# Kernel optimization log

Hardware: AMD Instinct MI355X
Metric: run time of the kernel (lower is better)

Reference implementation:

```python
import jax, jax.numpy as jnp
import numpy as np

K = 40        # nearest neighbors
BN_EPS = 1e-5  # nn.BatchNorm1d default eps


def _bn(x, g, b):
    # training-mode BatchNorm1d: batch mean, biased variance
    mu = x.mean(0)
    var = x.var(0)
    return g * (x - mu) / jnp.sqrt(var + BN_EPS) + b


def setup_inputs() -> dict:
    key = jax.random.key(0)
    ks = jax.random.split(key, 16)
    N, Cin, D, S, P = 8192, 16, 32, 3, 32

    def w(k, i, o):
        return jax.random.normal(k, (i, o), jnp.float32) * (1.0 / np.sqrt(i))

    return {
        "x": jax.random.normal(ks[0], (N, Cin), jnp.float32),
        "original_coords": jax.random.normal(ks[1], (N, 3), jnp.float32),
        "batch": jnp.zeros((N,), jnp.int32),
        "step_count": 0,
        "num_layer": 1,
        # pre_gravnet MLP
        "pre_w1": w(ks[2], Cin, D), "pre_b1": jnp.zeros((D,), jnp.float32),
        "pre_w2": w(ks[3], D, D), "pre_b2": jnp.zeros((D,), jnp.float32),
        "bn1_g": jnp.ones((D,), jnp.float32), "bn1_b": jnp.zeros((D,), jnp.float32),
        # GravNetConv projections
        "lin_s_w": w(ks[4], D, S),
        "lin_h_w": w(ks[5], D, P), "lin_h_b": jnp.zeros((P,), jnp.float32),
        "lin_w": w(ks[6], D + 2 * P, D), "lin_b": jnp.zeros((D,), jnp.float32),
        # post_gravnet MLP (in = out_channels + space_dims + d_shape = 32+3+32)
        "post_w1": w(ks[7], D + S + D, D), "post_b1": jnp.zeros((D,), jnp.float32),
        "post_w2": w(ks[8], D, D), "post_b2": jnp.zeros((D,), jnp.float32),
        "bn2_g": jnp.ones((D,), jnp.float32), "bn2_b": jnp.zeros((D,), jnp.float32),
    }


def reference(x, original_coords, batch, step_count, num_layer,
              pre_w1, pre_b1, pre_w2, pre_b2, bn1_g, bn1_b,
              lin_s_w, lin_h_w, lin_h_b, lin_w, lin_b,
              post_w1, post_b1, post_w2, post_b2, bn2_g, bn2_b):
    N = x.shape[0]

    # pre_gravnet MLP + batchnorm
    h = jax.nn.elu(x @ pre_w1 + pre_b1)
    h = jax.nn.elu(h @ pre_w2 + pre_b2)
    x_in = _bn(h, bn1_g, bn1_b)

    # GravNetConv projections
    h_l = x_in @ lin_h_w + lin_h_b          # [N, P] propagated features
    s_l = x_in @ lin_s_w                    # [N, S] learned coordinate space

    # kNN graph in s-space (self loops excluded)
    sq = jnp.sum(s_l * s_l, axis=1)
    d2 = sq[:, None] + sq[None, :] - 2.0 * (s_l @ s_l.T)   # [N, N]
    d2 = jnp.maximum(d2, 0.0)
    d2 = jnp.where(jnp.eye(N, dtype=bool), jnp.inf, d2)
    _, idx = jax.lax.top_k(-d2, K)           # [N, K] neighbor indices

    # per-edge squared distance (NOTE: propagate uses the SQUARED distance,
    # faithful to the source where edge_weight is never re-bound to sqrt)
    edge_sq = jnp.take_along_axis(d2, idx, axis=1)    # [N, K]
    dist = jnp.sqrt(edge_sq + 1e-6)                   # [N, K]

    # DGL-side reductions at dst = edge_index[1] = neighbor index
    dst = idx.reshape(-1)
    distf = dist.reshape(-1)
    indeg = jax.ops.segment_sum(jnp.ones_like(distf), dst, num_segments=N)
    sum_d = jax.ops.segment_sum(distf, dst, num_segments=N)
    avdist = jnp.where(indeg > 0, sum_d / jnp.maximum(indeg, 1.0), 0.0)
    loss_regularizing_neig = 0.01 * jnp.mean(jnp.square(avdist - 0.5))

    norm_d = distf / (sum_d + 1e-4)[dst]              # EdgeWeightNorm('right')
    # faithful to source bug: '_edge_w_gndist' is set to the NORMALIZED dist,
    # and apply_edges multiplies by the RAW '_edge_w'
    degs2 = jax.ops.segment_sum(norm_d, dst, num_segments=N) + 1e-4
    gn_final = distf / degs2[dst]
    loss_llregulariser = 0.1 * jnp.mean(jnp.square(norm_d - gn_final))

    # message passing: msg = h_l[neighbor] * squared_dist, mean+max over the
    # K neighbors of each source node (regular fan-in -> dense reduce)
    msgs = h_l[idx] * edge_sq[..., None]              # [N, K, P]
    agg = jnp.concatenate([msgs.mean(1), msgs.max(1)], axis=-1)  # [N, 2P]
    xgn = jnp.concatenate([agg, x_in], axis=-1) @ lin_w + lin_b   # [N, 32]

    # post_gravnet MLP + batchnorm
    cat = jnp.concatenate([xgn, s_l, x_in], axis=1)   # [N, 67]
    o = jax.nn.elu(cat @ post_w1 + post_b1)
    o = jax.nn.elu(o @ post_w2 + post_b2)
    out = _bn(o, bn2_g, bn2_b)
    return (out, loss_regularizing_neig, loss_llregulariser)
```

## Files before the change

kernel.cpp:

```cpp
#include <hip/hip_runtime.h>
#include <math.h>

#define NPTS 8192
#define KNN 40
#define DD 32
#define CIN 16
#define RPB 8
#define QPB 8
#define QTR 2048
#define CAP3 64

#define OFF_H      0u
#define OFF_XIN    262144u
#define OFF_HL     524288u
#define OFF_SL     786432u
#define OFF_ESQ    819200u
#define OFF_O      1146880u
#define OFF_IDX    1409024u
#define OFF_SUMD   1736704u
#define OFF_INDEG  1744896u
#define OFF_STATS  1753088u
#define ZERO_FLOATS (8192u + 8192u + 130u * 32u)

#define ST(i) stats[(i) * 32]

__device__ __forceinline__ float elu_f(float x) { return x > 0.f ? x : (expf(x) - 1.f); }

__device__ __forceinline__ float grp_sum32(float v) {
#pragma unroll
    for (int m = 1; m < 32; m <<= 1) v += __shfl_xor(v, m);
    return v;
}

__device__ __forceinline__ unsigned fkey(float x) {
    unsigned b = __float_as_uint(x);
    return b ^ ((unsigned)((int)b >> 31) | 0x80000000u);
}
__device__ __forceinline__ float kinv(unsigned k) {
    unsigned b = (k & 0x80000000u) ? (k ^ 0x80000000u) : ~k;
    return __uint_as_float(b);
}

__device__ __forceinline__ unsigned bisect_kth4(unsigned u0, unsigned u1,
    unsigned u2, unsigned u3, int kth) {
    unsigned lo = 0u, hi = 0xFFFFFFFFu;
    while (lo < hi) {
        unsigned mid = lo + ((hi - lo) >> 1);
        int cnt = __popcll(__ballot(u0 <= mid)) + __popcll(__ballot(u1 <= mid))
                + __popcll(__ballot(u2 <= mid)) + __popcll(__ballot(u3 <= mid));
        if (cnt >= kth) hi = mid; else lo = mid + 1;
    }
    return hi;
}

__global__ __launch_bounds__(256) void k_pre(const float* __restrict__ x,
    const float* __restrict__ w1, const float* __restrict__ b1,
    const float* __restrict__ w2, const float* __restrict__ b2,
    float* __restrict__ h, float* __restrict__ stats)
{
    __shared__ float sw1[CIN * DD], sw2[DD * DD], sb1[DD], sb2[DD];
    __shared__ float bufx[RPB][20], buft[RPB][36];
    __shared__ float sstat[2 * DD];
    int tid = threadIdx.x;
    for (int t = tid; t < CIN * DD; t += 256) sw1[t] = w1[t];
    for (int t = tid; t < DD * DD; t += 256) sw2[t] = w2[t];
    if (tid < DD) { sb1[tid] = b1[tid]; sb2[tid] = b2[tid]; }
    if (tid < 2 * DD) sstat[tid] = 0.f;

    int r = tid >> 5, ch = tid & 31;
    int g = blockIdx.x * RPB + r;
    if (ch < CIN) bufx[r][ch] = x[(size_t)g * CIN + ch];
    __syncthreads();

    float acc = sb1[ch];
#pragma unroll
    for (int k4 = 0; k4 < CIN; k4 += 4) {
        float4 v = *(const float4*)&bufx[r][k4];
        acc = fmaf(v.x, sw1[(k4 + 0) * DD + ch], acc);
        acc = fmaf(v.y, sw1[(k4 + 1) * DD + ch], acc);
        acc = fmaf(v.z, sw1[(k4 + 2) * DD + ch], acc);
        acc = fmaf(v.w, sw1[(k4 + 3) * DD + ch], acc);
    }
    acc = elu_f(acc);
    buft[r][ch] = acc;
    __syncthreads();

    float o = sb2[ch];
#pragma unroll
    for (int k4 = 0; k4 < DD; k4 += 4) {
        float4 v = *(const float4*)&buft[r][k4];
        o = fmaf(v.x, sw2[(k4 + 0) * DD + ch], o);
        o = fmaf(v.y, sw2[(k4 + 1) * DD + ch], o);
        o = fmaf(v.z, sw2[(k4 + 2) * DD + ch], o);
        o = fmaf(v.w, sw2[(k4 + 3) * DD + ch], o);
    }
    o = elu_f(o);
    h[(size_t)g * DD + ch] = o;

    float s = o + __shfl_xor(o, 32);
    float q = o * o;
    q += __shfl_xor(q, 32);
    if ((tid & 32) == 0) { atomicAdd(&sstat[ch], s); atomicAdd(&sstat[DD + ch], q); }
    __syncthreads();
    if (tid < 2 * DD) atomicAdd(&ST(tid), sstat[tid]);
}

__global__ __launch_bounds__(256) void k_proj(const float* __restrict__ h,
    const float* __restrict__ stats,
    const float* __restrict__ g1, const float* __restrict__ b1g,
    const float* __restrict__ hw, const float* __restrict__ hb,
    const float* __restrict__ sw,
    float* __restrict__ xin, float* __restrict__ hl, float4* __restrict__ sl4)
{
    __shared__ float shw[DD * DD], ssw[DD * 3], sa[DD], sbp[DD], shb[DD];
    __shared__ float rrow[RPB][36];
    int tid = threadIdx.x;
    for (int t = tid; t < DD * DD; t += 256) shw[t] = hw[t];
    if (tid < DD * 3) ssw[tid] = sw[tid];
    if (tid < DD) {
        float mean = ST(tid) * (1.f / NPTS);
        float var = ST(32 + tid) * (1.f / NPTS) - mean * mean;
        float a = g1[tid] * rsqrtf(var + 1e-5f);
        sa[tid] = a;
        sbp[tid] = b1g[tid] - a * mean;
        shb[tid] = hb[tid];
    }
    __syncthreads();

    int r = tid >> 5, ch = tid & 31;
    int g = blockIdx.x * RPB + r;

    float v = fmaf(sa[ch], h[(size_t)g * DD + ch], sbp[ch]);
    xin[(size_t)g * DD + ch] = v;
    rrow[r][ch] = v;

    float p0 = v * ssw[ch * 3 + 0];
    float p1 = v * ssw[ch * 3 + 1];
    float p2 = v * ssw[ch * 3 + 2];
    p0 = grp_sum32(p0); p1 = grp_sum32(p1); p2 = grp_sum32(p2);
    if (ch == 0) sl4[g] = make_float4(p0, p1, p2, 0.5f * (p0 * p0 + p1 * p1 + p2 * p2));
    __syncthreads();

    float o = shb[ch];
#pragma unroll
    for (int k4 = 0; k4 < DD; k4 += 4) {
        float4 vv = *(const float4*)&rrow[r][k4];
        o = fmaf(vv.x, shw[(k4 + 0) * DD + ch], o);
        o = fmaf(vv.y, shw[(k4 + 1) * DD + ch], o);
        o = fmaf(vv.z, shw[(k4 + 2) * DD + ch], o);
        o = fmaf(vv.w, shw[(k4 + 3) * DD + ch], o);
    }
    hl[(size_t)g * DD + ch] = o;
}

__device__ __forceinline__ void emit_one(unsigned u, int j, float qw,
    unsigned thr, int nlt, int need, int prelt, int preeq,
    unsigned long long mlt, unsigned long long meq, unsigned long long ltm,
    int rb, int* __restrict__ idxo, float* __restrict__ esq,
    float* __restrict__ sumd, float* __restrict__ indeg)
{
    int pos = -1;
    if (u < thr) pos = prelt + __popcll(mlt & ltm);
    else if (u == thr) {
        int rk = preeq + __popcll(meq & ltm);
        if (rk < need) pos = nlt + rk;
    }
    if (pos >= 0) {
        float e = kinv(u);
        float d2 = fmaxf(2.f * (e + qw), 0.f);
        idxo[rb + pos] = j; esq[rb + pos] = d2;
        float dist = sqrtf(d2 + 1e-6f);
        atomicAdd(&sumd[j], dist); atomicAdd(&indeg[j], 1.f);
    }
}

__device__ __forceinline__ void select_emit4(
    const float2* b0, int c0, const float2* b1, int c1,
    const float2* b2, int c2, const float2* b3, int c3,
    int qidx, float qw, int lane,
    int* __restrict__ idxo, float* __restrict__ esq,
    float* __restrict__ sumd, float* __restrict__ indeg)
{
    float e0 = INFINITY, e1 = INFINITY, e2 = INFINITY, e3 = INFINITY;
    int j0 = -1, j1 = -1, j2 = -1, j3 = -1;
    if (lane < c0) { float2 t = b0[lane]; e0 = t.x; j0 = __float_as_int(t.y); }
    if (lane < c1) { float2 t = b1[lane]; e1 = t.x; j1 = __float_as_int(t.y); }
    if (lane < c2) { float2 t = b2[lane]; e2 = t.x; j2 = __float_as_int(t.y); }
    if (lane < c3) { float2 t = b3[lane]; e3 = t.x; j3 = __float_as_int(t.y); }
    if (j0 == qidx) e0 = INFINITY;
    if (j1 == qidx) e1 = INFINITY;
    if (j2 == qidx) e2 = INFINITY;
    if (j3 == qidx) e3 = INFINITY;
    unsigned u0 = fkey(e0), u1 = fkey(e1), u2 = fkey(e2), u3 = fkey(e3);
    unsigned thr = bisect_kth4(u0, u1, u2, u3, KNN);
    unsigned long long ltm = (1ull << lane) - 1;
    unsigned long long mlt0 = __ballot(u0 < thr), mlt1 = __ballot(u1 < thr);
    unsigned long long mlt2 = __ballot(u2 < thr), mlt3 = __ballot(u3 < thr);
    unsigned long long meq0 = __ballot(u0 == thr), meq1 = __ballot(u1 == thr);
    unsigned long long meq2 = __ballot(u2 == thr), meq3 = __ballot(u3 == thr);
    int n0 = __popcll(mlt0), n1 = __popcll(mlt1), n2 = __popcll(mlt2), n3 = __popcll(mlt3);
    int q0 = __popcll(meq0), q1 = __popcll(meq1), q2 = __popcll(meq2);
    int nlt = n0 + n1 + n2 + n3;
    int need = KNN - nlt;
    int rb = qidx * KNN;

    emit_one(u0, j0, qw, thr, nlt, need, 0, 0, mlt0, meq0, ltm, rb, idxo, esq, sumd, indeg);
    emit_one(u1, j1, qw, thr, nlt, need, n0, q0, mlt1, meq1, ltm, rb, idxo, esq, sumd, indeg);
    emit_one(u2, j2, qw, thr, nlt, need, n0 + n1, q0 + q1, mlt2, meq2, ltm, rb, idxo, esq, sumd, indeg);
    emit_one(u3, j3, qw, thr, nlt, need, n0 + n1 + n2, q0 + q1 + q2, mlt3, meq3, ltm, rb, idxo, esq, sumd, indeg);
}

#define EDIST8(pt, q) fmaf(-qx[q], (pt).x, fmaf(-qy[q], (pt).y, fmaf(-qz[q], (pt).z, (pt).w)))

__global__ __launch_bounds__(256) void k_knn(const float4* __restrict__ sl4,
    int* __restrict__ idxo, float* __restrict__ esq,
    float* __restrict__ sumd, float* __restrict__ indeg)
{
    __shared__ float pool[QPB][4][64];
    __shared__ float2 cand[QPB][4][CAP3];
    __shared__ int cnts[QPB][4];
    __shared__ float sthr[QPB];
    int tid = threadIdx.x, lane = tid & 63, w = tid >> 6;
    int qbase = blockIdx.x * QPB;

    float qx[QPB], qy[QPB], qz[QPB];
#pragma unroll
    for (int q = 0; q < QPB; ++q) {
        float4 t = sl4[qbase + q];
        qx[q] = t.x; qy[q] = t.y; qz[q] = t.z;
    }
    int pbase = w * QTR;
    int rot = blockIdx.x & (QTR / 64 - 1);

    float m0[QPB];
#pragma unroll
    for (int q = 0; q < QPB; ++q) m0[q] = INFINITY;

    for (int i = 0; i < QTR / 64; ++i) {
        int chunk = (i + rot) & (QTR / 64 - 1);
        float4 pt = sl4[pbase + chunk * 64 + lane];
#pragma unroll
        for (int q = 0; q < QPB; ++q) m0[q] = fminf(m0[q], EDIST8(pt, q));
    }
#pragma unroll
    for (int q = 0; q < QPB; ++q) pool[q][w][lane] = m0[q];
    __syncthreads();

#pragma unroll
    for (int k = 0; k < 2; ++k) {
        int q = 2 * w + k;
        unsigned t = bisect_kth4(fkey(pool[q][0][lane]), fkey(pool[q][1][lane]),
                                 fkey(pool[q][2][lane]), fkey(pool[q][3][lane]), KNN + 1);
        if (lane == 0) sthr[q] = kinv(t);
    }
    __syncthreads();

    float thr[QPB];
#pragma unroll
    for (int q = 0; q < QPB; ++q) thr[q] = sthr[q];

    unsigned long long ltm = (1ull << lane) - 1;
    int cnt[QPB];
#pragma unroll
    for (int q = 0; q < QPB; ++q) cnt[q] = 0;

    for (int i = 0; i < QTR / 64; ++i) {
        int chunk = (i + rot) & (QTR / 64 - 1);
        int jj = pbase + chunk * 64 + lane;
        float4 pt = sl4[jj];
#pragma unroll
        for (int q = 0; q < QPB; ++q) {
            float e = EDIST8(pt, q);
            unsigned long long mm = __ballot(e <= thr[q]);
            if (mm) {
                if (e <= thr[q]) {
                    int pos = cnt[q] + __popcll(mm & ltm);
                    if (pos < CAP3) cand[q][w][pos] = make_float2(e, __int_as_float(jj));
                }
                cnt[q] += __popcll(mm);
            }
        }
    }
    if (lane == 0) {
#pragma unroll
        for (int q = 0; q < QPB; ++q) cnts[q][w] = cnt[q] < CAP3 ? cnt[q] : CAP3;
    }
    __syncthreads();

#pragma unroll
    for (int k = 0; k < 2; ++k) {
        int q = 2 * w + k;
        int qi = qbase + q;
        float qw_ = sl4[qi].w;
        select_emit4(cand[q][0], cnts[q][0], cand[q][1], cnts[q][1],
                     cand[q][2], cnts[q][2], cand[q][3], cnts[q][3],
                     qi, qw_, lane, idxo, esq, sumd, indeg);
    }
}

__global__ __launch_bounds__(256) void k_agg(
    const int* __restrict__ idx, const float* __restrict__ esq,
    const float* __restrict__ hl, const float* __restrict__ xin,
    const float4* __restrict__ sl4,
    const float* __restrict__ sumd, const float* __restrict__ indeg,
    const float* __restrict__ lw, const float* __restrict__ lb,
    const float* __restrict__ pw1, const float* __restrict__ pb1,
    const float* __restrict__ pw2, const float* __restrict__ pb2,
    float* __restrict__ o, float* __restrict__ stats)
{
    __shared__ float slw[96 * DD], spw1[67 * DD], spw2[DD * DD];
    __shared__ float slb[DD], spb1[DD], spb2[DD];
    __shared__ float rbuf[RPB][100];
    __shared__ float rb2[RPB][68];
    __shared__ float sstat[2 * DD];
    __shared__ float sl1, sl2;
    int tid = threadIdx.x;
    for (int t = tid; t < 96 * DD; t += 256) slw[t] = lw[t];
    for (int t = tid; t < 67 * DD; t += 256) spw1[t] = pw1[t];
    for (int t = tid; t < DD * DD; t += 256) spw2[t] = pw2[t];
    if (tid < DD) { slb[tid] = lb[tid]; spb1[tid] = pb1[tid]; spb2[tid] = pb2[tid]; }
    if (tid < 2 * DD) sstat[tid] = 0.f;
    if (tid == 254) sl1 = 0.f;
    if (tid == 255) sl2 = 0.f;

    int r = tid >> 5, ch = tid & 31;
    int g = blockIdx.x * RPB + r;
    int rb = g * KNN;

    float sv = 0.f, mv = -INFINITY;
#pragma unroll 8
    for (int k = 0; k < KNN; ++k) {
        int j = idx[rb + k];
        float w = esq[rb + k];
        float m = hl[(size_t)j * DD + ch] * w;
        sv += m;
        mv = fmaxf(mv, m);
    }
    rbuf[r][ch] = sv * (1.f / KNN);
    rbuf[r][32 + ch] = mv;
    rbuf[r][64 + ch] = xin[(size_t)g * DD + ch];
    if (ch == 0) { float4 s = sl4[g]; rbuf[r][96] = s.x; rbuf[r][97] = s.y; rbuf[r][98] = s.z; }
    __syncthreads();

    float l2 = 0.f;
    {
        int j = idx[rb + ch];
        float w = esq[rb + ch];
        float dist = sqrtf(w + 1e-6f);
        float sd = sumd[j];
        float r1 = 1.f / (sd + 1e-4f);
        float dg = sd * r1 + 1e-4f;
        float df = dist * r1 - dist / dg;
        l2 = df * df;
        if (ch < KNN - 32) {
            j = idx[rb + 32 + ch];
            w = esq[rb + 32 + ch];
            dist = sqrtf(w + 1e-6f);
            sd = sumd[j];
            r1 = 1.f / (sd + 1e-4f);
            dg = sd * r1 + 1e-4f;
            df = dist * r1 - dist / dg;
            l2 += df * df;
        }
    }
    l2 = grp_sum32(l2);
    if (ch == 0) {
        float id = indeg[g], sdg = sumd[g];
        float av = id > 0.f ? sdg / fmaxf(id, 1.f) : 0.f;
        float dd = av - 0.5f;
        atomicAdd(&sl2, l2);
        atomicAdd(&sl1, dd * dd);
    }

    float acc = slb[ch];
#pragma unroll
    for (int k4 = 0; k4 < 96; k4 += 4) {
        float4 v = *(const float4*)&rbuf[r][k4];
        acc = fmaf(v.x, slw[(k4 + 0) * DD + ch], acc);
        acc = fmaf(v.y, slw[(k4 + 1) * DD + ch], acc);
        acc = fmaf(v.z, slw[(k4 + 2) * DD + ch], acc);
        acc = fmaf(v.w, slw[(k4 + 3) * DD + ch], acc);
    }
    rb2[r][ch] = acc;
    __syncthreads();

    acc = spb1[ch];
#pragma unroll
    for (int k4 = 0; k4 < DD; k4 += 4) {
        float4 v = *(const float4*)&rb2[r][k4];
        acc = fmaf(v.x, spw1[(k4 + 0) * DD + ch], acc);
        acc = fmaf(v.y, spw1[(k4 + 1) * DD + ch], acc);
        acc = fmaf(v.z, spw1[(k4 + 2) * DD + ch], acc);
        acc = fmaf(v.w, spw1[(k4 + 3) * DD + ch], acc);
    }
#pragma unroll
    for (int s2 = 0; s2 < 3; ++s2)
        acc = fmaf(rbuf[r][96 + s2], spw1[(32 + s2) * DD + ch], acc);
#pragma unroll
    for (int k4 = 0; k4 < DD; k4 += 4) {
        float4 v = *(const float4*)&rbuf[r][64 + k4];
        acc = fmaf(v.x, spw1[(35 + k4 + 0) * DD + ch], acc);
        acc = fmaf(v.y, spw1[(35 + k4 + 1) * DD + ch], acc);
        acc = fmaf(v.z, spw1[(35 + k4 + 2) * DD + ch], acc);
        acc = fmaf(v.w, spw1[(35 + k4 + 3) * DD + ch], acc);
    }
    acc = elu_f(acc);
    rb2[r][32 + ch] = acc;
    __syncthreads();

    acc = spb2[ch];
#pragma unroll
    for (int k4 = 0; k4 < DD; k4 += 4) {
        float4 v = *(const float4*)&rb2[r][32 + k4];
        acc = fmaf(v.x, spw2[(k4 + 0) * DD + ch], acc);
        acc = fmaf(v.y, spw2[(k4 + 1) * DD + ch], acc);
        acc = fmaf(v.z, spw2[(k4 + 2) * DD + ch], acc);
        acc = fmaf(v.w, spw2[(k4 + 3) * DD + ch], acc);
    }
    acc = elu_f(acc);
    o[(size_t)g * DD + ch] = acc;

    float s = acc + __shfl_xor(acc, 32);
    float q = acc * acc;
    q += __shfl_xor(q, 32);
    if ((tid & 32) == 0) { atomicAdd(&sstat[ch], s); atomicAdd(&sstat[DD + ch], q); }
    __syncthreads();
    if (tid < 2 * DD) atomicAdd(&ST(64 + tid), sstat[tid]);
    if (tid == 0) { atomicAdd(&ST(128), sl1); atomicAdd(&ST(129), sl2); }
}

__global__ __launch_bounds__(256) void k_out(const float* __restrict__ o,
    const float* __restrict__ stats, const float* __restrict__ g,
    const float* __restrict__ b, float* __restrict__ dout)
{
    __shared__ float sa[DD], sb[DD];
    int tid = threadIdx.x;
    if (tid < DD) {
        float mean = ST(64 + tid) * (1.f / NPTS);
        float var = ST(96 + tid) * (1.f / NPTS) - mean * mean;
        float a = g[tid] * rsqrtf(var + 1e-5f);
        sa[tid] = a;
        sb[tid] = b[tid] - a * mean;
    }
    __syncthreads();

    int t = blockIdx.x * 256 + tid;
    float4 v = ((const float4*)o)[t];
    int cbase = (t * 4) & (DD - 1);
    float4 rr;
    rr.x = fmaf(sa[cbase + 0], v.x, sb[cbase + 0]);
    rr.y = fmaf(sa[cbase + 1], v.y, sb[cbase + 1]);
    rr.z = fmaf(sa[cbase + 2], v.z, sb[cbase + 2]);
    rr.w = fmaf(sa[cbase + 3], v.w, sb[cbase + 3]);
    ((float4*)dout)[t] = rr;

    if (blockIdx.x == 0) {
        if (tid == DD)     dout[NPTS * DD]     = 0.01f * ST(128) * (1.f / NPTS);
        if (tid == DD + 1) dout[NPTS * DD + 1] = 0.1f  * ST(129) * (1.f / ((float)NPTS * KNN));
    }
}

extern "C" void kernel_launch(void* const* d_in, const int* in_sizes, int n_in,
                              void* d_out, int out_size, void* d_ws, size_t ws_size,
                              hipStream_t stream)
{
    (void)in_sizes; (void)n_in; (void)out_size; (void)ws_size;
    const float* x      = (const float*)d_in[0];
    const float* pre_w1 = (const float*)d_in[5];
    const float* pre_b1 = (const float*)d_in[6];
    const float* pre_w2 = (const float*)d_in[7];
    const float* pre_b2 = (const float*)d_in[8];
    const float* bn1_g  = (const float*)d_in[9];
    const float* bn1_b  = (const float*)d_in[10];
    const float* lin_s_w = (const float*)d_in[11];
    const float* lin_h_w = (const float*)d_in[12];
    const float* lin_h_b = (const float*)d_in[13];
    const float* lin_w   = (const float*)d_in[14];
    const float* lin_b   = (const float*)d_in[15];
    const float* post_w1 = (const float*)d_in[16];
    const float* post_b1 = (const float*)d_in[17];
    const float* post_w2 = (const float*)d_in[18];
    const float* post_b2 = (const float*)d_in[19];
    const float* bn2_g   = (const float*)d_in[20];
    const float* bn2_b   = (const float*)d_in[21];

    float* W = (float*)d_ws;
    float* h     = W + OFF_H;
    float* xin   = W + OFF_XIN;
    float* hl    = W + OFF_HL;
    float4* sl4  = (float4*)(W + OFF_SL);
    float* esq   = W + OFF_ESQ;
    float* o     = W + OFF_O;
    int*   idx   = (int*)(W + OFF_IDX);
    float* sumd  = W + OFF_SUMD;
    float* indeg = W + OFF_INDEG;
    float* stats = W + OFF_STATS;
    float* dout  = (float*)d_out;

    hipMemsetAsync(W + OFF_SUMD, 0, ZERO_FLOATS * sizeof(float), stream);

    k_pre<<<NPTS / RPB, 256, 0, stream>>>(x, pre_w1, pre_b1, pre_w2, pre_b2, h, stats);
    k_proj<<<NPTS / RPB, 256, 0, stream>>>(h, stats, bn1_g, bn1_b,
                                           lin_h_w, lin_h_b, lin_s_w, xin, hl, sl4);
    k_knn<<<NPTS / QPB, 256, 0, stream>>>(sl4, idx, esq, sumd, indeg);
    k_agg<<<NPTS / RPB, 256, 0, stream>>>(idx, esq, hl, xin, sl4, sumd, indeg,
                                          lin_w, lin_b, post_w1, post_b1, post_w2, post_b2,
                                          o, stats);
    k_out<<<NPTS * DD / 1024, 256, 0, stream>>>(o, stats, bn2_g, bn2_b, dout);
}
```

Baseline: 122.9 us.

## Split kNN point scan across eight waves per block with one query per wave

The kNN kernel now launches 512 threads per block, so eight wavefronts each scan one eighth of the points for the block's eight queries instead of four wavefronts scanning a quarter. Each wave then handles threshold bisection and final selection for one query over eight candidate pools of 32 entries, where before each wave handled two queries over four pools of 64. Query coordinates and thresholds are made wave-uniform with readfirstlane so they can sit in scalar registers. This halves the serial scan per wave, but a per-wave candidate cap of 32 is easier to overflow on clustered data, and the block needs more registers and LDS.

Measured after the change: 123.3 us. About the same (+0.3%).

```diff
diff --git a/kernel.cpp b/kernel.cpp
--- a/kernel.cpp
+++ b/kernel.cpp
@@ -7,8 +7,8 @@
 #define CIN 16
 #define RPB 8
 #define QPB 8
-#define QTR 2048
-#define CAP3 64
+#define EIGHTH (NPTS / 8)
+#define CAPQ 32
 
 #define OFF_H      0u
 #define OFF_XIN    262144u
@@ -30,6 +30,10 @@
 #pragma unroll
     for (int m = 1; m < 32; m <<= 1) v += __shfl_xor(v, m);
     return v;
+}
+
+__device__ __forceinline__ float rfl(float v) {
+    return __int_as_float(__builtin_amdgcn_readfirstlane(__float_as_int(v)));
 }
 
 __device__ __forceinline__ unsigned fkey(float x) {
@@ -174,51 +178,13 @@
     }
 }
 
-__device__ __forceinline__ void select_emit4(
-    const float2* b0, int c0, const float2* b1, int c1,
-    const float2* b2, int c2, const float2* b3, int c3,
-    int qidx, float qw, int lane,
+__global__ __launch_bounds__(512, 8) void k_knn(const float4* __restrict__ sl4,
     int* __restrict__ idxo, float* __restrict__ esq,
     float* __restrict__ sumd, float* __restrict__ indeg)
 {
-    float e0 = INFINITY, e1 = INFINITY, e2 = INFINITY, e3 = INFINITY;
-    int j0 = -1, j1 = -1, j2 = -1, j3 = -1;
-    if (lane < c0) { float2 t = b0[lane]; e0 = t.x; j0 = __float_as_int(t.y); }
-    if (lane < c1) { float2 t = b1[lane]; e1 = t.x; j1 = __float_as_int(t.y); }
-    if (lane < c2) { float2 t = b2[lane]; e2 = t.x; j2 = __float_as_int(t.y); }
-    if (lane < c3) { float2 t = b3[lane]; e3 = t.x; j3 = __float_as_int(t.y); }
-    if (j0 == qidx) e0 = INFINITY;
-    if (j1 == qidx) e1 = INFINITY;
-    if (j2 == qidx) e2 = INFINITY;
-    if (j3 == qidx) e3 = INFINITY;
-    unsigned u0 = fkey(e0), u1 = fkey(e1), u2 = fkey(e2), u3 = fkey(e3);
-    unsigned thr = bisect_kth4(u0, u1, u2, u3, KNN);
-    unsigned long long ltm = (1ull << lane) - 1;
-    unsigned long long mlt0 = __ballot(u0 < thr), mlt1 = __ballot(u1 < thr);
-    unsigned long long mlt2 = __ballot(u2 < thr), mlt3 = __ballot(u3 < thr);
-    unsigned long long meq0 = __ballot(u0 == thr), meq1 = __ballot(u1 == thr);
-    unsigned long long meq2 = __ballot(u2 == thr), meq3 = __ballot(u3 == thr);
-    int n0 = __popcll(mlt0), n1 = __popcll(mlt1), n2 = __popcll(mlt2), n3 = __popcll(mlt3);
-    int q0 = __popcll(meq0), q1 = __popcll(meq1), q2 = __popcll(meq2);
-    int nlt = n0 + n1 + n2 + n3;
-    int need = KNN - nlt;
-    int rb = qidx * KNN;
-
-    emit_one(u0, j0, qw, thr, nlt, need, 0, 0, mlt0, meq0, ltm, rb, idxo, esq, sumd, indeg);
-    emit_one(u1, j1, qw, thr, nlt, need, n0, q0, mlt1, meq1, ltm, rb, idxo, esq, sumd, indeg);
-    emit_one(u2, j2, qw, thr, nlt, need, n0 + n1, q0 + q1, mlt2, meq2, ltm, rb, idxo, esq, sumd, indeg);
-    emit_one(u3, j3, qw, thr, nlt, need, n0 + n1 + n2, q0 + q1 + q2, mlt3, meq3, ltm, rb, idxo, esq, sumd, indeg);
-}
-
-#define EDIST8(pt, q) fmaf(-qx[q], (pt).x, fmaf(-qy[q], (pt).y, fmaf(-qz[q], (pt).z, (pt).w)))
-
-__global__ __launch_bounds__(256) void k_knn(const float4* __restrict__ sl4,
-    int* __restrict__ idxo, float* __restrict__ esq,
-    float* __restrict__ sumd, float* __restrict__ indeg)
-{
-    __shared__ float pool[QPB][4][64];
-    __shared__ float2 cand[QPB][4][CAP3];
-    __shared__ int cnts[QPB][4];
+    __shared__ float pool[QPB][8][64];
+    __shared__ float2 cand[QPB][8][CAPQ];
+    __shared__ int cnts[QPB][8];
     __shared__ float sthr[QPB];
     int tid = threadIdx.x, lane = tid & 63, w = tid >> 6;
     int qbase = blockIdx.x * QPB;
@@ -227,55 +193,67 @@
 #pragma unroll
     for (int q = 0; q < QPB; ++q) {
         float4 t = sl4[qbase + q];
-        qx[q] = t.x; qy[q] = t.y; qz[q] = t.z;
-    }
-    int pbase = w * QTR;
-    int rot = blockIdx.x & (QTR / 64 - 1);
+        qx[q] = rfl(t.x); qy[q] = rfl(t.y); qz[q] = rfl(t.z);
+    }
+    int pbase = w * EIGHTH;
+    int rot = blockIdx.x & (EIGHTH / 64 - 1);
 
     float m0[QPB];
 #pragma unroll
     for (int q = 0; q < QPB; ++q) m0[q] = INFINITY;
 
-    for (int i = 0; i < QTR / 64; ++i) {
-        int chunk = (i + rot) & (QTR / 64 - 1);
+    for (int i = 0; i < EIGHTH / 64; ++i) {
+        int chunk = (i + rot) & (EIGHTH / 64 - 1);
         float4 pt = sl4[pbase + chunk * 64 + lane];
 #pragma unroll
-        for (int q = 0; q < QPB; ++q) m0[q] = fminf(m0[q], EDIST8(pt, q));
+        for (int q = 0; q < QPB; ++q) {
+            float e = fmaf(-qx[q], pt.x, fmaf(-qy[q], pt.y, fmaf(-qz[q], pt.z, pt.w)));
+            m0[q] = fminf(m0[q], e);
+        }
     }
 #pragma unroll
     for (int q = 0; q < QPB; ++q) pool[q][w][lane] = m0[q];
     __syncthreads();
 
-#pragma unroll
-    for (int k = 0; k < 2; ++k) {
-        int q = 2 * w + k;
-        unsigned t = bisect_kth4(fkey(pool[q][0][lane]), fkey(pool[q][1][lane]),
-                                 fkey(pool[q][2][lane]), fkey(pool[q][3][lane]), KNN + 1);
-        if (lane == 0) sthr[q] = kinv(t);
+    {
+        unsigned u0 = fkey(pool[w][0][lane]), u1 = fkey(pool[w][1][lane]);
+        unsigned u2 = fkey(pool[w][2][lane]), u3 = fkey(pool[w][3][lane]);
+        unsigned u4 = fkey(pool[w][4][lane]), u5 = fkey(pool[w][5][lane]);
+        unsigned u6 = fkey(pool[w][6][lane]), u7 = fkey(pool[w][7][lane]);
+        unsigned lo = 0u, hi = 0xFFFFFFFFu;
+        while (lo < hi) {
+            unsigned mid = lo + ((hi - lo) >> 1);
+            int c = __popcll(__ballot(u0 <= mid)) + __popcll(__ballot(u1 <= mid))
+                  + __popcll(__ballot(u2 <= mid)) + __popcll(__ballot(u3 <= mid))
+                  + __popcll(__ballot(u4 <= mid)) + __popcll(__ballot(u5 <= mid))
+                  + __popcll(__ballot(u6 <= mid)) + __popcll(__ballot(u7 <= mid));
+            if (c >= KNN + 1) hi = mid; else lo = mid + 1;
+        }
+        if (lane == 0) sthr[w] = kinv(hi);
     }
     __syncthreads();
 
     float thr[QPB];
 #pragma unroll
-    for (int q = 0; q < QPB; ++q) thr[q] = sthr[q];
+    for (int q = 0; q < QPB; ++q) thr[q] = rfl(sthr[q]);
 
     unsigned long long ltm = (1ull << lane) - 1;
     int cnt[QPB];
 #pragma unroll
     for (int q = 0; q < QPB; ++q) cnt[q] = 0;
 
-    for (int i = 0; i < QTR / 64; ++i) {
-        int chunk = (i + rot) & (QTR / 64 - 1);
+    for (int i = 0; i < EIGHTH / 64; ++i) {
+        int chunk = (i + rot) & (EIGHTH / 64 - 1);
         int jj = pbase + chunk * 64 + lane;
         float4 pt = sl4[jj];
 #pragma unroll
         for (int q = 0; q < QPB; ++q) {
-            float e = EDIST8(pt, q);
+            float e = fmaf(-qx[q], pt.x, fmaf(-qy[q], pt.y, fmaf(-qz[q], pt.z, pt.w)));
             unsigned long long mm = __ballot(e <= thr[q]);
             if (mm) {
                 if (e <= thr[q]) {
                     int pos = cnt[q] + __popcll(mm & ltm);
-                    if (pos < CAP3) cand[q][w][pos] = make_float2(e, __int_as_float(jj));
+                    if (pos < CAPQ) cand[q][w][pos] = make_float2(e, __int_as_float(jj));
                 }
                 cnt[q] += __popcll(mm);
             }
@@ -283,19 +261,39 @@
     }
     if (lane == 0) {
 #pragma unroll
-        for (int q = 0; q < QPB; ++q) cnts[q][w] = cnt[q] < CAP3 ? cnt[q] : CAP3;
-    }
-    __syncthreads();
-
-#pragma unroll
-    for (int k = 0; k < 2; ++k) {
-        int q = 2 * w + k;
-        int qi = qbase + q;
-        float qw_ = sl4[qi].w;
-        select_emit4(cand[q][0], cnts[q][0], cand[q][1], cnts[q][1],
-                     cand[q][2], cnts[q][2], cand[q][3], cnts[q][3],
-                     qi, qw_, lane, idxo, esq, sumd, indeg);
-    }
+        for (int q = 0; q < QPB; ++q) cnts[q][w] = cnt[q] < CAPQ ? cnt[q] : CAPQ;
+    }
+    __syncthreads();
+
+    int qi = qbase + w;
+    float qw_ = sl4[qi].w;
+    float ev[4]; int jv[4];
+#pragma unroll
+    for (int s = 0; s < 4; ++s) {
+        int slot = s * 64 + lane;
+        int e8 = slot >> 5, ii = slot & 31;
+        float2 t = cand[w][e8][ii];
+        bool valid = ii < cnts[w][e8];
+        float e = valid ? t.x : INFINITY;
+        int j = valid ? __float_as_int(t.y) : -1;
+        if (j == qi) e = INFINITY;
+        ev[s] = e; jv[s] = j;
+    }
+    unsigned u0 = fkey(ev[0]), u1 = fkey(ev[1]), u2 = fkey(ev[2]), u3 = fkey(ev[3]);
+    unsigned thr2 = bisect_kth4(u0, u1, u2, u3, KNN);
+    unsigned long long mlt0 = __ballot(u0 < thr2), mlt1 = __ballot(u1 < thr2);
+    unsigned long long mlt2 = __ballot(u2 < thr2), mlt3 = __ballot(u3 < thr2);
+    unsigned long long meq0 = __ballot(u0 == thr2), meq1 = __ballot(u1 == thr2);
+    unsigned long long meq2 = __ballot(u2 == thr2), meq3 = __ballot(u3 == thr2);
+    int n0 = __popcll(mlt0), n1 = __popcll(mlt1), n2 = __popcll(mlt2), n3 = __popcll(mlt3);
+    int q0c = __popcll(meq0), q1c = __popcll(meq1), q2c = __popcll(meq2);
+    int nlt = n0 + n1 + n2 + n3;
+    int need = KNN - nlt;
+    int rb = qi * KNN;
+    emit_one(u0, jv[0], qw_, thr2, nlt, need, 0, 0, mlt0, meq0, ltm, rb, idxo, esq, sumd, indeg);
+    emit_one(u1, jv[1], qw_, thr2, nlt, need, n0, q0c, mlt1, meq1, ltm, rb, idxo, esq, sumd, indeg);
+    emit_one(u2, jv[2], qw_, thr2, nlt, need, n0 + n1, q0c + q1c, mlt2, meq2, ltm, rb, idxo, esq, sumd, indeg);
+    emit_one(u3, jv[3], qw_, thr2, nlt, need, n0 + n1 + n2, q0c + q1c + q2c, mlt3, meq3, ltm, rb, idxo, esq, sumd, indeg);
 }
 
 __global__ __launch_bounds__(256) void k_agg(
@@ -502,7 +500,7 @@
     k_pre<<<NPTS / RPB, 256, 0, stream>>>(x, pre_w1, pre_b1, pre_w2, pre_b2, h, stats);
     k_proj<<<NPTS / RPB, 256, 0, stream>>>(h, stats, bn1_g, bn1_b,
                                            lin_h_w, lin_h_b, lin_s_w, xin, hl, sl4);
-    k_knn<<<NPTS / QPB, 256, 0, stream>>>(sl4, idx, esq, sumd, indeg);
+    k_knn<<<NPTS / QPB, 512, 0, stream>>>(sl4, idx, esq, sumd, indeg);
     k_agg<<<NPTS / RPB, 256, 0, stream>>>(idx, esq, hl, xin, sl4, sumd, indeg,
                                           lin_w, lin_b, post_w1, post_b1, post_w2, post_b2,
                                           o, stats);
```
